# Kernel optimization log

Hardware: AMD Instinct MI355X
Metric: run time of the kernel (lower is better)

Reference implementation:

```python
import jax, jax.numpy as jnp
import numpy as np

NUM_GROUPS = 32
EPS = 1e-6


def group_norm(x, gamma, beta):
    # x: [B, C, H, W]
    b, c, h, w = x.shape
    xg = x.reshape(b, NUM_GROUPS, c // NUM_GROUPS, h, w)
    mean = xg.mean(axis=(2, 3, 4), keepdims=True)
    var = xg.var(axis=(2, 3, 4), keepdims=True)
    xn = ((xg - mean) * jax.lax.rsqrt(var + EPS)).reshape(b, c, h, w)
    return xn * gamma[None, :, None, None] + beta[None, :, None, None]


def setup_inputs() -> dict:
    key = jax.random.key(0)
    ks = jax.random.split(key, 10)
    B, C, H, W = 2, 512, 64, 64
    s = 1.0 / np.sqrt(C)
    return {
        "x": jax.random.normal(ks[0], (B, C, H, W), dtype=jnp.float32),
        "gamma": jnp.ones((C,), jnp.float32),
        "beta": jnp.zeros((C,), jnp.float32),
        "Wq": jax.random.normal(ks[1], (C, C), jnp.float32) * s,
        "bq": jnp.zeros((C,), jnp.float32),
        "Wk": jax.random.normal(ks[2], (C, C), jnp.float32) * s,
        "bk": jnp.zeros((C,), jnp.float32),
        "Wv": jax.random.normal(ks[3], (C, C), jnp.float32) * s,
        "bv": jnp.zeros((C,), jnp.float32),
        "Wo": jax.random.normal(ks[4], (C, C), jnp.float32) * s,
        "bo": jnp.zeros((C,), jnp.float32),
    }


def reference(x, gamma, beta, Wq, bq, Wk, bk, Wv, bv, Wo, bo):
    b, c, h, w = x.shape
    hn = group_norm(x, gamma, beta)               # [B,C,H,W]
    hf = hn.reshape(b, c, h * w)                  # [B,C,N]
    # 1x1 convs == channel matmuls
    q = jnp.einsum('oc,bcn->bon', Wq, hf) + bq[None, :, None]
    k = jnp.einsum('oc,bcn->bon', Wk, hf) + bk[None, :, None]
    v = jnp.einsum('oc,bcn->bon', Wv, hf) + bv[None, :, None]
    scale = float(c) ** -0.5
    scores = jnp.einsum('bci,bcj->bij', q, k) * scale   # [B,N,N]
    attn = jax.nn.softmax(scores, axis=-1)
    out = jnp.einsum('bij,bcj->bci', attn, v)            # [B,C,N]
    out = jnp.einsum('oc,bcn->bon', Wo, out) + bo[None, :, None]
    return x + out.reshape(b, c, h, w)
```

## Files before the change

### kernel.cpp

```cpp
#include <hip/hip_runtime.h>

#define BB 2
#define CC 512
#define NS 4096
#define NGROUP 32
#define TILE 128
#define RSTRIDE 132

typedef __bf16 bf16_8 __attribute__((ext_vector_type(8)));
typedef __bf16 bf16_4 __attribute__((ext_vector_type(4)));
typedef float f32_4 __attribute__((ext_vector_type(4)));

#define SMEM_BYTES 65536

__device__ __forceinline__ void gld_lds16(const __bf16* g, __bf16* l) {
  __builtin_amdgcn_global_load_lds(
      (const __attribute__((address_space(1))) unsigned int*)g,
      (__attribute__((address_space(3))) unsigned int*)l, 16, 0, 0);
}

__global__ __launch_bounds__(256) void gn_stats(const float* __restrict__ x,
                                                float* __restrict__ stats) {
  const float4* p = (const float4*)(x + (size_t)blockIdx.x * 65536);
  float s = 0.f, q = 0.f;
  for (int i = threadIdx.x; i < 16384; i += 256) {
    float4 v = p[i];
    s += v.x + v.y + v.z + v.w;
    q += v.x * v.x + v.y * v.y + v.z * v.z + v.w * v.w;
  }
#pragma unroll
  for (int off = 32; off > 0; off >>= 1) {
    s += __shfl_down(s, off, 64);
    q += __shfl_down(q, off, 64);
  }
  __shared__ float ls[4], lq[4];
  int wave = threadIdx.x >> 6, lane = threadIdx.x & 63;
  if (lane == 0) { ls[wave] = s; lq[wave] = q; }
  __syncthreads();
  if (threadIdx.x == 0) {
    float S = ls[0] + ls[1] + ls[2] + ls[3];
    float Q = lq[0] + lq[1] + lq[2] + lq[3];
    float mean = S * (1.f / 65536.f);
    float var = Q * (1.f / 65536.f) - mean * mean;
    stats[blockIdx.x * 2] = mean;
    stats[blockIdx.x * 2 + 1] = rsqrtf(var + 1e-6f);
  }
}

__global__ __launch_bounds__(256) void gn_apply_t(const float* __restrict__ x,
                                                  const float* __restrict__ stats,
                                                  const float* __restrict__ gamma,
                                                  const float* __restrict__ beta,
                                                  __bf16* __restrict__ hnT) {
  __shared__ float tile[32][33];
  int b = blockIdx.z;
  int c0 = blockIdx.y * 32;
  int n0 = blockIdx.x * 32;
  int tx = threadIdx.x;
  int ty = threadIdx.y;
  const float* xb = x + (size_t)b * CC * NS;
#pragma unroll
  for (int i = 0; i < 4; i++) {
    int c = c0 + ty + i * 8;
    float mean = stats[(b * NGROUP + (c >> 4)) * 2 + 0];
    float rstd = stats[(b * NGROUP + (c >> 4)) * 2 + 1];
    float v = xb[(size_t)c * NS + n0 + tx];
    tile[ty + i * 8][tx] = (v - mean) * rstd * gamma[c] + beta[c];
  }
  __syncthreads();
  __bf16* out = hnT + (size_t)b * NS * CC;
#pragma unroll
  for (int i = 0; i < 4; i++) {
    int n = n0 + ty + i * 8;
    out[(size_t)n * CC + c0 + tx] = (__bf16)tile[tx][ty + i * 8];
  }
}

__global__ __launch_bounds__(256) void cvt_w(const float* __restrict__ w0, const float* __restrict__ w1,
                                             const float* __restrict__ w2, const float* __restrict__ w3,
                                             __bf16* __restrict__ o0, __bf16* __restrict__ o1,
                                             __bf16* __restrict__ o2, __bf16* __restrict__ o3) {
  int tsel = blockIdx.x >> 8;
  int i = (blockIdx.x & 255) * 256 + threadIdx.x;
  const float* src = tsel == 0 ? w0 : tsel == 1 ? w1 : tsel == 2 ? w2 : w3;
  __bf16* dst = tsel == 0 ? o0 : tsel == 1 ? o1 : tsel == 2 ? o2 : o3;
  float4 v = ((const float4*)src)[i];
  bf16_4 r;
  r[0] = (__bf16)v.x; r[1] = (__bf16)v.y; r[2] = (__bf16)v.z; r[3] = (__bf16)v.w;
  ((bf16_4*)dst)[i] = r;
}

__device__ __forceinline__ void gemm_core8(const __bf16* __restrict__ A, const __bf16* __restrict__ B,
                                           int K, int lda, int ldb,
                                           __bf16* lds, f32_4 (&acc)[4][2]) {
  const int t = threadIdx.x;
  const int lane = t & 63;
  const int wave = t >> 6;
  const int lrow = lane & 15, quad = lane >> 4;
  const int wrow = (wave >> 2) * 64, wcol = (wave & 3) * 32;
  const int co = (quad ^ ((lrow >> 1) & 3)) * 8;
  const int r0 = t >> 2;
  const int kp = ((t & 3) ^ ((t >> 3) & 3)) * 8;
  const __bf16* pA = A + (size_t)r0 * lda + kp;
  const __bf16* pB = B + (size_t)r0 * ldb + kp;
  {
    __bf16* lA = lds;
    __bf16* lB = lds + 8192;
    gld_lds16(pA,      &lA[t * 8]);
    gld_lds16(pA + 32, &lA[4096 + t * 8]);
    gld_lds16(pB,      &lB[t * 8]);
    gld_lds16(pB + 32, &lB[4096 + t * 8]);
  }
  int buf = 0;
  for (int k0 = 0; k0 < K; k0 += 64, buf ^= 1) {
    __syncthreads();
    if (k0 + 64 < K) {
      __bf16* lA = lds + (buf ^ 1) * 16384;
      __bf16* lB = lA + 8192;
      gld_lds16(pA + k0 + 64, &lA[t * 8]);
      gld_lds16(pA + k0 + 96, &lA[4096 + t * 8]);
      gld_lds16(pB + k0 + 64, &lB[t * 8]);
      gld_lds16(pB + k0 + 96, &lB[4096 + t * 8]);
    }
    const __bf16* bA = lds + buf * 16384;
    const __bf16* bB = bA + 8192;
#pragma unroll
    for (int ks = 0; ks < 2; ks++) {
      const __bf16* la = bA + ks * 4096;
      const __bf16* lb = bB + ks * 4096;
      bf16_8 af[4], bfr[2];
#pragma unroll
      for (int i = 0; i < 4; i++)
        af[i] = *(const bf16_8*)&la[(wrow + i * 16 + lrow) * 32 + co];
#pragma unroll
      for (int j = 0; j < 2; j++)
        bfr[j] = *(const bf16_8*)&lb[(wcol + j * 16 + lrow) * 32 + co];
#pragma unroll
      for (int i = 0; i < 4; i++)
#pragma unroll
        for (int j = 0; j < 2; j++)
          acc[i][j] = __builtin_amdgcn_mfma_f32_16x16x32_bf16(af[i], bfr[j], acc[i][j], 0, 0, 0);
    }
  }
}

__device__ __forceinline__ void stage_acc8(float* ls, const f32_4 (&acc)[4][2], int pass) {
  const int t = threadIdx.x;
  const int lane = t & 63, wave = t >> 6;
  const int lrow = lane & 15, quad = lane >> 4;
  const int wrow = (wave >> 2) * 64, wcol = (wave & 3) * 32;
  if ((wrow >> 6) == pass) {
#pragma unroll
    for (int i = 0; i < 4; i++)
#pragma unroll
      for (int r = 0; r < 4; r++)
#pragma unroll
        for (int jj = 0; jj < 2; jj++)
          ls[(i * 16 + quad * 4 + r) * RSTRIDE + wcol + jj * 16 + lrow] = acc[i][jj][r];
  }
}

__device__ __forceinline__ void drain_bf16_8(const float* ls, __bf16* gdst, int ldg) {
  const int t = threadIdx.x;
#pragma unroll
  for (int k2 = 0; k2 < 4; k2++) {
    int idx = k2 * 512 + t;
    int row = idx >> 5, col = (idx & 31) * 4;
    f32_4 v = *(const f32_4*)&ls[row * RSTRIDE + col];
    bf16_4 o;
    o[0] = (__bf16)v[0]; o[1] = (__bf16)v[1]; o[2] = (__bf16)v[2]; o[3] = (__bf16)v[3];
    *(bf16_4*)&gdst[(size_t)row * ldg + col] = o;
  }
}

__device__ __forceinline__ void gemm_core4(const __bf16* __restrict__ A, const __bf16* __restrict__ B,
                                           int K, int lda, int ldb,
                                           __bf16* lds, f32_4 (&acc)[4][4]) {
  const int t = threadIdx.x;
  const int lane = t & 63;
  const int wave = t >> 6;
  const int lrow = lane & 15, quad = lane >> 4;
  const int wrow = (wave >> 1) * 64, wcol = (wave & 1) * 64;
  const int co = (quad ^ ((lrow >> 1) & 3)) * 8;
  const int r0 = t >> 2;
  const int kp = ((t & 3) ^ ((t >> 3) & 3)) * 8;
  const __bf16* pA0 = A + (size_t)r0 * lda + kp;
  const __bf16* pA1 = A + (size_t)(r0 + 64) * lda + kp;
  const __bf16* pB0 = B + (size_t)r0 * ldb + kp;
  const __bf16* pB1 = B + (size_t)(r0 + 64) * ldb + kp;
  {
    __bf16* lA = lds;
    __bf16* lB = lds + 8192;
    gld_lds16(pA0,      &lA[t * 8]);
    gld_lds16(pA1,      &lA[2048 + t * 8]);
    gld_lds16(pA0 + 32, &lA[4096 + t * 8]);
    gld_lds16(pA1 + 32, &lA[6144 + t * 8]);
    gld_lds16(pB0,      &lB[t * 8]);
    gld_lds16(pB1,      &lB[2048 + t * 8]);
    gld_lds16(pB0 + 32, &lB[4096 + t * 8]);
    gld_lds16(pB1 + 32, &lB[6144 + t * 8]);
  }
  int buf = 0;
  for (int k0 = 0; k0 < K; k0 += 64, buf ^= 1) {
    __syncthreads();
    if (k0 + 64 < K) {
      __bf16* lA = lds + (buf ^ 1) * 16384;
      __bf16* lB = lA + 8192;
      gld_lds16(pA0 + k0 + 64, &lA[t * 8]);
      gld_lds16(pA1 + k0 + 64, &lA[2048 + t * 8]);
      gld_lds16(pA0 + k0 + 96, &lA[4096 + t * 8]);
      gld_lds16(pA1 + k0 + 96, &lA[6144 + t * 8]);
      gld_lds16(pB0 + k0 + 64, &lB[t * 8]);
      gld_lds16(pB1 + k0 + 64, &lB[2048 + t * 8]);
      gld_lds16(pB0 + k0 + 96, &lB[4096 + t * 8]);
      gld_lds16(pB1 + k0 + 96, &lB[6144 + t * 8]);
    }
    const __bf16* bA = lds + buf * 16384;
    const __bf16* bB = bA + 8192;
#pragma unroll
    for (int ks = 0; ks < 2; ks++) {
      const __bf16* la = bA + ks * 4096;
      const __bf16* lb = bB + ks * 4096;
      bf16_8 af[4], bfr[4];
#pragma unroll
      for (int i = 0; i < 4; i++)
        af[i] = *(const bf16_8*)&la[(wrow + i * 16 + lrow) * 32 + co];
#pragma unroll
      for (int j = 0; j < 4; j++)
        bfr[j] = *(const bf16_8*)&lb[(wcol + j * 16 + lrow) * 32 + co];
#pragma unroll
      for (int i = 0; i < 4; i++)
#pragma unroll
        for (int j = 0; j < 4; j++)
          acc[i][j] = __builtin_amdgcn_mfma_f32_16x16x32_bf16(af[i], bfr[j], acc[i][j], 0, 0, 0);
    }
  }
}

__global__ __launch_bounds__(512, 4) void qkv_gemm(const __bf16* __restrict__ hnT,
                                                   const __bf16* __restrict__ Wq,
                                                   const __bf16* __restrict__ Wk,
                                                   const __bf16* __restrict__ Wv,
                                                   const float* __restrict__ bq,
                                                   const float* __restrict__ bk,
                                                   const float* __restrict__ bv,
                                                   __bf16* __restrict__ qT,
                                                   __bf16* __restrict__ kT,
                                                   __bf16* __restrict__ vv) {
  __shared__ char smem[SMEM_BYTES];
  __bf16* lds = (__bf16*)smem;
  float* lsr = (float*)smem;
  const int b = blockIdx.z;
  const int id = blockIdx.x;
  const int sel = id >> 7;
  const int r = id & 127;
  const long long sBNC = (long long)NS * CC;
  const long long sBCN = (long long)CC * NS;

  int m0, n0, N;
  const __bf16 *Ap, *Bp;
  __bf16* Cp;
  const float* bias;
  if (sel < 2) {
    m0 = (r >> 2) * TILE;
    n0 = (r & 3) * TILE;
    Ap = hnT + (size_t)b * sBNC + (size_t)m0 * CC;
    Bp = (sel == 0 ? Wq : Wk) + (size_t)n0 * CC;
    Cp = (sel == 0 ? qT : kT) + (size_t)b * sBNC;
    bias = (sel == 0 ? bq : bk);
    N = CC;
  } else {
    m0 = (r & 3) * TILE;
    n0 = (r >> 2) * TILE;
    Ap = Wv + (size_t)m0 * CC;
    Bp = hnT + (size_t)b * sBNC + (size_t)n0 * CC;
    Cp = vv + (size_t)b * sBCN;
    bias = bv;
    N = NS;
  }

  f32_4 acc[4][2];
#pragma unroll
  for (int i = 0; i < 4; i++)
#pragma unroll
    for (int j = 0; j < 2; j++) acc[i][j] = {0.f, 0.f, 0.f, 0.f};

  gemm_core8(Ap, Bp, CC, CC, CC, lds, acc);

  const int t = threadIdx.x;
  const int lane = t & 63;
  const int lrow = lane & 15, quad = lane >> 4;
  const int wave = t >> 6;
  const int wrow = (wave >> 2) * 64, wcol = (wave & 3) * 32;
#pragma unroll
  for (int i = 0; i < 4; i++)
#pragma unroll
    for (int r2 = 0; r2 < 4; r2++) {
      float rowb = (sel == 2) ? bias[m0 + wrow + i * 16 + quad * 4 + r2] : 0.f;
#pragma unroll
      for (int j = 0; j < 2; j++) {
        float cb = (sel < 2) ? bias[n0 + wcol + j * 16 + lrow] : rowb;
        acc[i][j][r2] += cb;
      }
    }

#pragma unroll
  for (int p = 0; p < 2; p++) {
    __syncthreads();
    stage_acc8(lsr, acc, p);
    __syncthreads();
    drain_bf16_8(lsr, Cp + (size_t)(m0 + p * 64) * N + n0, N);
  }
}

__global__ __launch_bounds__(256) void e_gemm(const __bf16* __restrict__ qT,
                                              const __bf16* __restrict__ kT,
                                              __bf16* __restrict__ E,
                                              float* __restrict__ l,
                                              float scale) {
  __shared__ char smem[SMEM_BYTES];
  __bf16* lds = (__bf16*)smem;
  const int g = blockIdx.x;
  const int j = g & 7;
  const int b = j & 1;
  const int moct = j >> 1;
  const int k = g >> 3;
  const int sc = k >> 6;
  const int rem = k & 63;
  const int m0 = (moct * 8 + (rem >> 3)) * TILE;
  const int n0 = (sc * 8 + (rem & 7)) * TILE;
  const long long sBNC = (long long)NS * CC;
  const long long sBNN = (long long)NS * NS;
  const __bf16* Ap = qT + (size_t)b * sBNC + (size_t)m0 * CC;
  const __bf16* Bp = kT + (size_t)b * sBNC + (size_t)n0 * CC;

  f32_4 acc[4][4];
#pragma unroll
  for (int i = 0; i < 4; i++)
#pragma unroll
    for (int jj = 0; jj < 4; jj++) acc[i][jj] = {0.f, 0.f, 0.f, 0.f};

  gemm_core4(Ap, Bp, CC, CC, CC, lds, acc);

  const int t = threadIdx.x;
  const int lane = t & 63;
  const int lrow = lane & 15, quad = lane >> 4;
  const int wave = t >> 6;
  const int wrow = (wave >> 1) * 64, wcol = (wave & 1) * 64;
  __bf16* Ep = E + (size_t)b * sBNN;
  float* lp = l + (size_t)b * NS;
#pragma unroll
  for (int i = 0; i < 4; i++) {
#pragma unroll
    for (int r = 0; r < 4; r++) {
      int gm = m0 + wrow + i * 16 + quad * 4 + r;
      float rp = 0.f;
#pragma unroll
      for (int jj = 0; jj < 4; jj++) {
        int gn = n0 + wcol + jj * 16 + lrow;
        float ev = __expf(acc[i][jj][r] * scale);
        rp += ev;
        Ep[(size_t)gm * NS + gn] = (__bf16)ev;
      }
      rp += __shfl_down(rp, 8, 16);
      rp += __shfl_down(rp, 4, 16);
      rp += __shfl_down(rp, 2, 16);
      rp += __shfl_down(rp, 1, 16);
      if (lrow == 0) atomicAdd(&lp[gm], rp);
    }
  }
}

__global__ __launch_bounds__(512, 4) void ao_split4(const __bf16* __restrict__ E,
                                                    const __bf16* __restrict__ vv,
                                                    __bf16* __restrict__ p0,
                                                    __bf16* __restrict__ p1,
                                                    __bf16* __restrict__ p2,
                                                    __bf16* __restrict__ p3) {
  __shared__ char smem[SMEM_BYTES];
  __bf16* lds = (__bf16*)smem;
  float* lsr = (float*)smem;
  const int g = blockIdx.x;
  const int j = g & 7;
  const int b = j & 1;
  const int split = j >> 1;
  const int k = g >> 3;
  const int m0 = (k >> 2) * TILE;
  const int n0 = (k & 3) * TILE;
  const long long sBNN = (long long)NS * NS;
  const long long sBCN = (long long)CC * NS;
  const long long sBNC = (long long)NS * CC;
  const __bf16* Ap = E + (size_t)b * sBNN + (size_t)m0 * NS + (size_t)split * 1024;
  const __bf16* Bp = vv + (size_t)b * sBCN + (size_t)n0 * NS + (size_t)split * 1024;
  __bf16* Cp = (split == 0 ? p0 : split == 1 ? p1 : split == 2 ? p2 : p3) + (size_t)b * sBNC;

  f32_4 acc[4][2];
#pragma unroll
  for (int i = 0; i < 4; i++)
#pragma unroll
    for (int jj = 0; jj < 2; jj++) acc[i][jj] = {0.f, 0.f, 0.f, 0.f};

  gemm_core8(Ap, Bp, 1024, NS, NS, lds, acc);

#pragma unroll
  for (int p = 0; p < 2; p++) {
    __syncthreads();
    stage_acc8(lsr, acc, p);
    __syncthreads();
    drain_bf16_8(lsr, Cp + (size_t)(m0 + p * 64) * CC + n0, CC);
  }
}

__global__ __launch_bounds__(256) void reduce_ao4(const __bf16* __restrict__ p0,
                                                  const __bf16* __restrict__ p1,
                                                  const __bf16* __restrict__ p2,
                                                  const __bf16* __restrict__ p3,
                                                  const float* __restrict__ l,
                                                  __bf16* __restrict__ o) {
  int i = blockIdx.x * 256 + threadIdx.x;
  int row = i >> 6;
  float inv = 1.f / l[row];
  bf16_8 a = ((const bf16_8*)p0)[i];
  bf16_8 c = ((const bf16_8*)p1)[i];
  bf16_8 d = ((const bf16_8*)p2)[i];
  bf16_8 e = ((const bf16_8*)p3)[i];
  bf16_8 r;
#pragma unroll
  for (int k = 0; k < 8; k++)
    r[k] = (__bf16)(((float)a[k] + (float)c[k] + (float)d[k] + (float)e[k]) * inv);
  ((bf16_8*)o)[i] = r;
}

__global__ __launch_bounds__(512, 4) void wo_split(const __bf16* __restrict__ Wo,
                                                   const __bf16* __restrict__ aoT,
                                                   __bf16* __restrict__ pw0,
                                                   __bf16* __restrict__ pw1) {
  __shared__ char smem[SMEM_BYTES];
  __bf16* lds = (__bf16*)smem;
  float* lsr = (float*)smem;
  const int b = blockIdx.z & 1;
  const int split = blockIdx.z >> 1;
  const int m0 = blockIdx.y * TILE;
  const int n0 = blockIdx.x * TILE;
  const long long sBNC = (long long)NS * CC;
  const long long sBCN = (long long)CC * NS;
  const __bf16* Ap = Wo + (size_t)m0 * CC + (size_t)split * 256;
  const __bf16* Bp = aoT + (size_t)b * sBNC + (size_t)n0 * CC + (size_t)split * 256;
  __bf16* Cp = (split ? pw1 : pw0) + (size_t)b * sBCN;

  f32_4 acc[4][2];
#pragma unroll
  for (int i = 0; i < 4; i++)
#pragma unroll
    for (int j = 0; j < 2; j++) acc[i][j] = {0.f, 0.f, 0.f, 0.f};

  gemm_core8(Ap, Bp, 256, CC, CC, lds, acc);

#pragma unroll
  for (int p = 0; p < 2; p++) {
    __syncthreads();
    stage_acc8(lsr, acc, p);
    __syncthreads();
    drain_bf16_8(lsr, Cp + (size_t)(m0 + p * 64) * NS + n0, NS);
  }
}

__global__ __launch_bounds__(256) void final_out(const __bf16* __restrict__ pw0,
                                                 const __bf16* __restrict__ pw1,
                                                 const float* __restrict__ bo,
                                                 const float* __restrict__ x,
                                                 float* __restrict__ out) {
  int i = blockIdx.x * 256 + threadIdx.x;
  int o = (i >> 10) & (CC - 1);
  float bias = bo[o];
  bf16_4 a = ((const bf16_4*)pw0)[i];
  bf16_4 c = ((const bf16_4*)pw1)[i];
  float4 xr = ((const float4*)x)[i];
  float4 r;
  r.x = (float)a[0] + (float)c[0] + bias + xr.x;
  r.y = (float)a[1] + (float)c[1] + bias + xr.y;
  r.z = (float)a[2] + (float)c[2] + bias + xr.z;
  r.w = (float)a[3] + (float)c[3] + bias + xr.w;
  ((float4*)out)[i] = r;
}

extern "C" void kernel_launch(void* const* d_in, const int* in_sizes, int n_in,
                              void* d_out, int out_size, void* d_ws, size_t ws_size,
                              hipStream_t stream) {
  const float* x = (const float*)d_in[0];
  const float* gamma = (const float*)d_in[1];
  const float* beta = (const float*)d_in[2];
  const float* Wq = (const float*)d_in[3];
  const float* bq = (const float*)d_in[4];
  const float* Wk = (const float*)d_in[5];
  const float* bk = (const float*)d_in[6];
  const float* Wv = (const float*)d_in[7];
  const float* bv = (const float*)d_in[8];
  const float* Wo = (const float*)d_in[9];
  const float* bo = (const float*)d_in[10];
  float* out = (float*)d_out;

  char* ws = (char*)d_ws;
  __bf16* hnT = (__bf16*)(ws + 0);
  __bf16* qT  = (__bf16*)(ws + 8388608);
  __bf16* kT  = (__bf16*)(ws + 16777216);
  __bf16* vv  = (__bf16*)(ws + 25165824);
  __bf16* aoT = (__bf16*)(ws + 33554432);
  __bf16* Eb  = (__bf16*)(ws + 41943040);
  __bf16* pw0 = (__bf16*)(ws + 41943040);
  __bf16* pw1 = (__bf16*)(ws + 50331648);
  __bf16* Wqb = (__bf16*)(ws + 109051904);
  __bf16* Wkb = (__bf16*)(ws + 109576192);
  __bf16* Wvb = (__bf16*)(ws + 110100480);
  __bf16* Wob = (__bf16*)(ws + 110624768);
  float* stats = (float*)(ws + 111149056);
  float* lsum = (float*)(ws + 109051904);
  __bf16* p0 = hnT;
  __bf16* p1 = qT;
  __bf16* p2 = kT;
  __bf16* p3 = aoT;

  const float scale = 0.044194173824159216f;

  cvt_w<<<1024, 256, 0, stream>>>(Wq, Wk, Wv, Wo, Wqb, Wkb, Wvb, Wob);
  gn_stats<<<BB * NGROUP, 256, 0, stream>>>(x, stats);
  gn_apply_t<<<dim3(NS / 32, CC / 32, BB), dim3(32, 8), 0, stream>>>(x, stats, gamma, beta, hnT);

  qkv_gemm<<<dim3(384, 1, BB), 512, 0, stream>>>(hnT, Wqb, Wkb, Wvb, bq, bk, bv, qT, kT, vv);

  hipMemsetAsync(lsum, 0, BB * NS * sizeof(float), stream);
  e_gemm<<<2048, 256, 0, stream>>>(qT, kT, Eb, lsum, scale);

  ao_split4<<<1024, 512, 0, stream>>>(Eb, vv, p0, p1, p2, p3);
  reduce_ao4<<<2048, 256, 0, stream>>>(p0, p1, p2, p3, lsum, aoT);

  wo_split<<<dim3(NS / TILE, CC / TILE, 2 * BB), 512, 0, stream>>>(Wob, aoT, pw0, pw1);
  final_out<<<4096, 256, 0, stream>>>(pw0, pw1, bo, x, out);
}
```

Measured before the change: 266.5 us.

## Use 256x256 tiles with phased MFMA scheduling for score and attention-V GEMMs

Replaces the 128x128 GEMM core used by the score GEMM and the attention-times-V GEMM with a 256x256-tile core. The new core runs 8 waves and uses 128KB of dynamic LDS with double buffering, staggered A/B prefetch, explicit barriers and raised wave priority around MFMA phases. Larger tiles are meant to cut global and LDS traffic per FLOP and hide load latency. In exchange, occupancy drops to about one block per CU, the AO grid shrinks to 256 blocks, and the AO epilogue now writes bf16 values straight to global memory instead of staging them through LDS for coalesced stores.

```diff
diff --git a/kernel.cpp b/kernel.cpp
--- a/kernel.cpp
+++ b/kernel.cpp
@@ -12,6 +12,7 @@
 typedef float f32_4 __attribute__((ext_vector_type(4)));
 
 #define SMEM_BYTES 65536
+#define SMEM256 131072
 
 __device__ __forceinline__ void gld_lds16(const __bf16* g, __bf16* l) {
   __builtin_amdgcn_global_load_lds(
@@ -173,66 +174,206 @@
   }
 }
 
-__device__ __forceinline__ void gemm_core4(const __bf16* __restrict__ A, const __bf16* __restrict__ B,
-                                           int K, int lda, int ldb,
-                                           __bf16* lds, f32_4 (&acc)[4][4]) {
+__device__ __forceinline__ void gemm_core256(const __bf16* __restrict__ A,
+                                             const __bf16* __restrict__ B,
+                                             int K, int lda, int ldb,
+                                             __bf16* lds, f32_4 (&acc)[8][4]) {
   const int t = threadIdx.x;
   const int lane = t & 63;
   const int wave = t >> 6;
   const int lrow = lane & 15, quad = lane >> 4;
-  const int wrow = (wave >> 1) * 64, wcol = (wave & 1) * 64;
-  const int co = (quad ^ ((lrow >> 1) & 3)) * 8;
+  const int wm = wave >> 2, wn = wave & 3;
   const int r0 = t >> 2;
   const int kp = ((t & 3) ^ ((t >> 3) & 3)) * 8;
-  const __bf16* pA0 = A + (size_t)r0 * lda + kp;
-  const __bf16* pA1 = A + (size_t)(r0 + 64) * lda + kp;
-  const __bf16* pB0 = B + (size_t)r0 * ldb + kp;
-  const __bf16* pB1 = B + (size_t)(r0 + 64) * ldb + kp;
-  {
-    __bf16* lA = lds;
-    __bf16* lB = lds + 8192;
-    gld_lds16(pA0,      &lA[t * 8]);
-    gld_lds16(pA1,      &lA[2048 + t * 8]);
-    gld_lds16(pA0 + 32, &lA[4096 + t * 8]);
-    gld_lds16(pA1 + 32, &lA[6144 + t * 8]);
-    gld_lds16(pB0,      &lB[t * 8]);
-    gld_lds16(pB1,      &lB[2048 + t * 8]);
-    gld_lds16(pB0 + 32, &lB[4096 + t * 8]);
-    gld_lds16(pB1 + 32, &lB[6144 + t * 8]);
-  }
-  int buf = 0;
-  for (int k0 = 0; k0 < K; k0 += 64, buf ^= 1) {
-    __syncthreads();
-    if (k0 + 64 < K) {
-      __bf16* lA = lds + (buf ^ 1) * 16384;
-      __bf16* lB = lA + 8192;
-      gld_lds16(pA0 + k0 + 64, &lA[t * 8]);
-      gld_lds16(pA1 + k0 + 64, &lA[2048 + t * 8]);
-      gld_lds16(pA0 + k0 + 96, &lA[4096 + t * 8]);
-      gld_lds16(pA1 + k0 + 96, &lA[6144 + t * 8]);
-      gld_lds16(pB0 + k0 + 64, &lB[t * 8]);
-      gld_lds16(pB1 + k0 + 64, &lB[2048 + t * 8]);
-      gld_lds16(pB0 + k0 + 96, &lB[4096 + t * 8]);
-      gld_lds16(pB1 + k0 + 96, &lB[6144 + t * 8]);
+  const __bf16* gA0 = A + (size_t)r0 * lda + kp;
+  const __bf16* gA1 = A + (size_t)(r0 + 128) * lda + kp;
+  const __bf16* gB0 = B + (size_t)r0 * ldb + kp;
+  const __bf16* gB1 = B + (size_t)(r0 + 128) * ldb + kp;
+  const int co = (quad ^ ((lrow >> 1) & 3)) * 8;
+  const int aoff = (wm * 128 + lrow) * 32 + co;
+  const int boff = 16384 + (wn * 64 + lrow) * 32 + co;
+  const int KT = K >> 6;
+
+#define STG(bufv, isB, srcp, hh, ktv)                                         \
+  {                                                                           \
+    __bf16* d_ = lds + (bufv) * 32768 + (isB) * 16384 + (hh) * 4096 + t * 8;  \
+    const __bf16* s_ = (srcp) + (ktv) * 64;                                   \
+    gld_lds16(s_, d_);                                                        \
+    gld_lds16(s_ + 32, d_ + 8192);                                            \
+  }
+#define LOAD_AF(IH)                                                           \
+  _Pragma("unroll") for (int i = 0; i < 4; i++)                               \
+      _Pragma("unroll") for (int ks = 0; ks < 2; ks++)                        \
+          af[i][ks] = *(const bf16_8*)&bb[aoff + ((IH) * 4 + i) * 512 + ks * 8192];
+#define LOAD_BV(J0)                                                           \
+  _Pragma("unroll") for (int j = 0; j < 2; j++)                               \
+      _Pragma("unroll") for (int ks = 0; ks < 2; ks++)                        \
+          bv[(J0) + j][ks] = *(const bf16_8*)&bb[boff + ((J0) + j) * 512 + ks * 8192];
+#define MFMA16(I0, J0)                                                        \
+  _Pragma("unroll") for (int ks = 0; ks < 2; ks++)                            \
+      _Pragma("unroll") for (int i = 0; i < 4; i++)                           \
+          _Pragma("unroll") for (int j = 0; j < 2; j++)                       \
+              acc[(I0) + i][(J0) + j] = __builtin_amdgcn_mfma_f32_16x16x32_bf16( \
+                  af[i][ks], bv[(J0) + j][ks], acc[(I0) + i][(J0) + j], 0, 0, 0);
+#define PHASE_BEGIN()                                                         \
+  __builtin_amdgcn_s_barrier();                                               \
+  asm volatile("s_waitcnt lgkmcnt(0)" ::: "memory");                          \
+  __builtin_amdgcn_sched_barrier(0);                                          \
+  __builtin_amdgcn_s_setprio(1);
+#define PHASE_END()                                                           \
+  __builtin_amdgcn_s_setprio(0);                                              \
+  __builtin_amdgcn_s_barrier();
+
+  STG(0, 0, gA0, 0, 0)
+  STG(0, 0, gA1, 1, 0)
+  STG(0, 1, gB0, 0, 0)
+  STG(0, 1, gB1, 1, 0)
+  STG(1, 1, gB0, 0, 1)
+  STG(1, 1, gB1, 1, 1)
+  asm volatile("s_waitcnt vmcnt(4)" ::: "memory");
+  __builtin_amdgcn_s_barrier();
+
+  for (int it = 0; it < (KT >> 1); ++it) {
+#pragma unroll
+    for (int h = 0; h < 2; ++h) {
+      const int kt = 2 * it + h;
+      const __bf16* bb = lds + h * 32768;
+      bf16_8 af[4][2], bv[4][2];
+      LOAD_AF(0)
+      LOAD_BV(0)
+      if (kt + 1 < KT) STG(h ^ 1, 0, gA0, 0, kt + 1)
+      PHASE_BEGIN()
+      MFMA16(0, 0)
+      PHASE_END()
+      LOAD_BV(2)
+      if (kt + 1 < KT) STG(h ^ 1, 0, gA1, 1, kt + 1)
+      PHASE_BEGIN()
+      MFMA16(0, 2)
+      PHASE_END()
+      LOAD_AF(1)
+      if (kt + 2 < KT) STG(h, 1, gB0, 0, kt + 2)
+      PHASE_BEGIN()
+      MFMA16(4, 0)
+      PHASE_END()
+      if (kt + 2 < KT) STG(h, 1, gB1, 1, kt + 2)
+      PHASE_BEGIN()
+      MFMA16(4, 2)
+      __builtin_amdgcn_s_setprio(0);
+      if (kt + 2 < KT) {
+        asm volatile("s_waitcnt vmcnt(4)" ::: "memory");
+      } else {
+        asm volatile("s_waitcnt vmcnt(0)" ::: "memory");
+      }
+      __builtin_amdgcn_s_barrier();
     }
-    const __bf16* bA = lds + buf * 16384;
-    const __bf16* bB = bA + 8192;
-#pragma unroll
-    for (int ks = 0; ks < 2; ks++) {
-      const __bf16* la = bA + ks * 4096;
-      const __bf16* lb = bB + ks * 4096;
-      bf16_8 af[4], bfr[4];
-#pragma unroll
-      for (int i = 0; i < 4; i++)
-        af[i] = *(const bf16_8*)&la[(wrow + i * 16 + lrow) * 32 + co];
-#pragma unroll
-      for (int j = 0; j < 4; j++)
-        bfr[j] = *(const bf16_8*)&lb[(wcol + j * 16 + lrow) * 32 + co];
-#pragma unroll
-      for (int i = 0; i < 4; i++)
-#pragma unroll
-        for (int j = 0; j < 4; j++)
-          acc[i][j] = __builtin_amdgcn_mfma_f32_16x16x32_bf16(af[i], bfr[j], acc[i][j], 0, 0, 0);
+  }
+#undef STG
+#undef LOAD_AF
+#undef LOAD_BV
+#undef MFMA16
+#undef PHASE_BEGIN
+#undef PHASE_END
+}
+
+__global__ __launch_bounds__(512, 2) void e_gemm256(const __bf16* __restrict__ qT,
+                                                    const __bf16* __restrict__ kT,
+                                                    __bf16* __restrict__ E,
+                                                    float* __restrict__ l,
+                                                    float scale) {
+  extern __shared__ __bf16 ldsdyn[];
+  const int bid = blockIdx.x;
+  const int lin = (bid & 7) * 64 + (bid >> 3);
+  const int b = lin >> 8;
+  const int rm = lin & 255;
+  const int R = rm >> 5, s = rm & 31;
+  const int mt = (R >> 2) * 8 + (s >> 2);
+  const int nt = (R & 3) * 4 + (s & 3);
+  const int m0 = mt * 256, n0 = nt * 256;
+  const long long sBNC = (long long)NS * CC;
+  const long long sBNN = (long long)NS * NS;
+  const __bf16* Ap = qT + (size_t)b * sBNC + (size_t)m0 * CC;
+  const __bf16* Bp = kT + (size_t)b * sBNC + (size_t)n0 * CC;
+
+  f32_4 acc[8][4];
+#pragma unroll
+  for (int i = 0; i < 8; i++)
+#pragma unroll
+    for (int j = 0; j < 4; j++) acc[i][j] = {0.f, 0.f, 0.f, 0.f};
+
+  gemm_core256(Ap, Bp, CC, CC, CC, ldsdyn, acc);
+
+  const int t = threadIdx.x;
+  const int lane = t & 63, wave = t >> 6;
+  const int lrow = lane & 15, quad = lane >> 4;
+  const int wm = wave >> 2, wn = wave & 3;
+  __bf16* Ep = E + (size_t)b * sBNN;
+  float* lp = l + (size_t)b * NS;
+#pragma unroll
+  for (int i = 0; i < 8; i++) {
+#pragma unroll
+    for (int r = 0; r < 4; r++) {
+      int gm = m0 + wm * 128 + i * 16 + quad * 4 + r;
+      float rp = 0.f;
+#pragma unroll
+      for (int j = 0; j < 4; j++) {
+        int gn = n0 + wn * 64 + j * 16 + lrow;
+        float ev = __expf(acc[i][j][r] * scale);
+        rp += ev;
+        Ep[(size_t)gm * NS + gn] = (__bf16)ev;
+      }
+      rp += __shfl_down(rp, 8, 16);
+      rp += __shfl_down(rp, 4, 16);
+      rp += __shfl_down(rp, 2, 16);
+      rp += __shfl_down(rp, 1, 16);
+      if (lrow == 0) atomicAdd(&lp[gm], rp);
+    }
+  }
+}
+
+__global__ __launch_bounds__(512, 2) void ao256(const __bf16* __restrict__ E,
+                                                const __bf16* __restrict__ vv,
+                                                __bf16* __restrict__ p0,
+                                                __bf16* __restrict__ p1,
+                                                __bf16* __restrict__ p2,
+                                                __bf16* __restrict__ p3) {
+  extern __shared__ __bf16 ldsdyn[];
+  const int bid = blockIdx.x;
+  const int lin = (bid & 7) * 32 + (bid >> 3);
+  const int split = lin >> 6;
+  const int rem = lin & 63;
+  const int b = rem >> 5;
+  const int mt = (rem & 31) >> 1;
+  const int nt = rem & 1;
+  const int m0 = mt * 256, n0 = nt * 256;
+  const long long sBNN = (long long)NS * NS;
+  const long long sBCN = (long long)CC * NS;
+  const long long sBNC = (long long)NS * CC;
+  const __bf16* Ap = E + (size_t)b * sBNN + (size_t)m0 * NS + (size_t)split * 1024;
+  const __bf16* Bp = vv + (size_t)b * sBCN + (size_t)n0 * NS + (size_t)split * 1024;
+  __bf16* Cp = (split == 0 ? p0 : split == 1 ? p1 : split == 2 ? p2 : p3) + (size_t)b * sBNC;
+
+  f32_4 acc[8][4];
+#pragma unroll
+  for (int i = 0; i < 8; i++)
+#pragma unroll
+    for (int j = 0; j < 4; j++) acc[i][j] = {0.f, 0.f, 0.f, 0.f};
+
+  gemm_core256(Ap, Bp, 1024, NS, NS, ldsdyn, acc);
+
+  const int t = threadIdx.x;
+  const int lane = t & 63, wave = t >> 6;
+  const int lrow = lane & 15, quad = lane >> 4;
+  const int wm = wave >> 2, wn = wave & 3;
+#pragma unroll
+  for (int i = 0; i < 8; i++) {
+#pragma unroll
+    for (int r = 0; r < 4; r++) {
+      int gm = m0 + wm * 128 + i * 16 + quad * 4 + r;
+#pragma unroll
+      for (int j = 0; j < 4; j++) {
+        int gn = n0 + wn * 64 + j * 16 + lrow;
+        Cp[(size_t)gm * CC + gn] = (__bf16)acc[i][j][r];
+      }
     }
   }
 }
@@ -313,104 +454,6 @@
   }
 }
 
-__global__ __launch_bounds__(256) void e_gemm(const __bf16* __restrict__ qT,
-                                              const __bf16* __restrict__ kT,
-                                              __bf16* __restrict__ E,
-                                              float* __restrict__ l,
-                                              float scale) {
-  __shared__ char smem[SMEM_BYTES];
-  __bf16* lds = (__bf16*)smem;
-  const int g = blockIdx.x;
-  const int j = g & 7;
-  const int b = j & 1;
-  const int moct = j >> 1;
-  const int k = g >> 3;
-  const int sc = k >> 6;
-  const int rem = k & 63;
-  const int m0 = (moct * 8 + (rem >> 3)) * TILE;
-  const int n0 = (sc * 8 + (rem & 7)) * TILE;
-  const long long sBNC = (long long)NS * CC;
-  const long long sBNN = (long long)NS * NS;
-  const __bf16* Ap = qT + (size_t)b * sBNC + (size_t)m0 * CC;
-  const __bf16* Bp = kT + (size_t)b * sBNC + (size_t)n0 * CC;
-
-  f32_4 acc[4][4];
-#pragma unroll
-  for (int i = 0; i < 4; i++)
-#pragma unroll
-    for (int jj = 0; jj < 4; jj++) acc[i][jj] = {0.f, 0.f, 0.f, 0.f};
-
-  gemm_core4(Ap, Bp, CC, CC, CC, lds, acc);
-
-  const int t = threadIdx.x;
-  const int lane = t & 63;
-  const int lrow = lane & 15, quad = lane >> 4;
-  const int wave = t >> 6;
-  const int wrow = (wave >> 1) * 64, wcol = (wave & 1) * 64;
-  __bf16* Ep = E + (size_t)b * sBNN;
-  float* lp = l + (size_t)b * NS;
-#pragma unroll
-  for (int i = 0; i < 4; i++) {
-#pragma unroll
-    for (int r = 0; r < 4; r++) {
-      int gm = m0 + wrow + i * 16 + quad * 4 + r;
-      float rp = 0.f;
-#pragma unroll
-      for (int jj = 0; jj < 4; jj++) {
-        int gn = n0 + wcol + jj * 16 + lrow;
-        float ev = __expf(acc[i][jj][r] * scale);
-        rp += ev;
-        Ep[(size_t)gm * NS + gn] = (__bf16)ev;
-      }
-      rp += __shfl_down(rp, 8, 16);
-      rp += __shfl_down(rp, 4, 16);
-      rp += __shfl_down(rp, 2, 16);
-      rp += __shfl_down(rp, 1, 16);
-      if (lrow == 0) atomicAdd(&lp[gm], rp);
-    }
-  }
-}
-
-__global__ __launch_bounds__(512, 4) void ao_split4(const __bf16* __restrict__ E,
-                                                    const __bf16* __restrict__ vv,
-                                                    __bf16* __restrict__ p0,
-                                                    __bf16* __restrict__ p1,
-                                                    __bf16* __restrict__ p2,
-                                                    __bf16* __restrict__ p3) {
-  __shared__ char smem[SMEM_BYTES];
-  __bf16* lds = (__bf16*)smem;
-  float* lsr = (float*)smem;
-  const int g = blockIdx.x;
-  const int j = g & 7;
-  const int b = j & 1;
-  const int split = j >> 1;
-  const int k = g >> 3;
-  const int m0 = (k >> 2) * TILE;
-  const int n0 = (k & 3) * TILE;
-  const long long sBNN = (long long)NS * NS;
-  const long long sBCN = (long long)CC * NS;
-  const long long sBNC = (long long)NS * CC;
-  const __bf16* Ap = E + (size_t)b * sBNN + (size_t)m0 * NS + (size_t)split * 1024;
-  const __bf16* Bp = vv + (size_t)b * sBCN + (size_t)n0 * NS + (size_t)split * 1024;
-  __bf16* Cp = (split == 0 ? p0 : split == 1 ? p1 : split == 2 ? p2 : p3) + (size_t)b * sBNC;
-
-  f32_4 acc[4][2];
-#pragma unroll
-  for (int i = 0; i < 4; i++)
-#pragma unroll
-    for (int jj = 0; jj < 2; jj++) acc[i][jj] = {0.f, 0.f, 0.f, 0.f};
-
-  gemm_core8(Ap, Bp, 1024, NS, NS, lds, acc);
-
-#pragma unroll
-  for (int p = 0; p < 2; p++) {
-    __syncthreads();
-    stage_acc8(lsr, acc, p);
-    __syncthreads();
-    drain_bf16_8(lsr, Cp + (size_t)(m0 + p * 64) * CC + n0, CC);
-  }
-}
-
 __global__ __launch_bounds__(256) void reduce_ao4(const __bf16* __restrict__ p0,
                                                   const __bf16* __restrict__ p1,
                                                   const __bf16* __restrict__ p2,
@@ -522,6 +565,15 @@
 
   const float scale = 0.044194173824159216f;
 
+  static int smem_attr_set = 0;
+  if (!smem_attr_set) {
+    hipFuncSetAttribute(reinterpret_cast<const void*>(e_gemm256),
+                        hipFuncAttributeMaxDynamicSharedMemorySize, SMEM256);
+    hipFuncSetAttribute(reinterpret_cast<const void*>(ao256),
+                        hipFuncAttributeMaxDynamicSharedMemorySize, SMEM256);
+    smem_attr_set = 1;
+  }
+
   cvt_w<<<1024, 256, 0, stream>>>(Wq, Wk, Wv, Wo, Wqb, Wkb, Wvb, Wob);
   gn_stats<<<BB * NGROUP, 256, 0, stream>>>(x, stats);
   gn_apply_t<<<dim3(NS / 32, CC / 32, BB), dim3(32, 8), 0, stream>>>(x, stats, gamma, beta, hnT);
@@ -529,9 +581,9 @@
   qkv_gemm<<<dim3(384, 1, BB), 512, 0, stream>>>(hnT, Wqb, Wkb, Wvb, bq, bk, bv, qT, kT, vv);
 
   hipMemsetAsync(lsum, 0, BB * NS * sizeof(float), stream);
-  e_gemm<<<2048, 256, 0, stream>>>(qT, kT, Eb, lsum, scale);
-
-  ao_split4<<<1024, 512, 0, stream>>>(Eb, vv, p0, p1, p2, p3);
+  e_gemm256<<<512, 512, SMEM256, stream>>>(qT, kT, Eb, lsum, scale);
+
+  ao256<<<256, 512, SMEM256, stream>>>(Eb, vv, p0, p1, p2, p3);
   reduce_ao4<<<2048, 256, 0, stream>>>(p0, p1, p2, p3, lsum, aoT);
 
   wo_split<<<dim3(NS / TILE, CC / TILE, 2 * BB), 512, 0, stream>>>(Wob, aoT, pw0, pw1);
```

Measured after the change: 246.8 us. 7.4% less time.
